# Kernel tuning notes

Hardware: AMD Instinct MI355X
Metric: run time of the kernel (lower is better)

The kernel has to match this reference:

```python
import jax, jax.numpy as jnp
import numpy as np

NUM_HEADS = 2

def mha(q, k, v, w_in, b_in, w_out, b_out):
    # torch nn.MultiheadAttention with batch_first=True, packed in_proj
    E = q.shape[-1]
    Dh = E // NUM_HEADS
    wq, wk, wv = jnp.split(w_in, 3, axis=0)
    bq, bk, bv = jnp.split(b_in, 3, axis=0)
    qh = (q @ wq.T + bq).reshape(q.shape[0], q.shape[1], NUM_HEADS, Dh)
    kh = (k @ wk.T + bk).reshape(k.shape[0], k.shape[1], NUM_HEADS, Dh)
    vh = (v @ wv.T + bv).reshape(v.shape[0], v.shape[1], NUM_HEADS, Dh)
    scores = jnp.einsum('blhd,bmhd->bhlm', qh, kh) / jnp.sqrt(jnp.asarray(Dh, q.dtype))
    attn = jax.nn.softmax(scores, axis=-1)
    ctx = jnp.einsum('bhlm,bmhd->blhd', attn, vh).reshape(q.shape[0], q.shape[1], E)
    return ctx @ w_out.T + b_out


def setup_inputs() -> dict:
    key = jax.random.key(0)
    ks = jax.random.split(key, 10)
    B, S, F, E, H = 16384, 512, 4, 8, 16
    s = 0.3
    return {
        'x': jax.random.normal(ks[0], (B, S, E), jnp.float32),
        'Q': jax.random.normal(ks[1], (F, E), jnp.float32) * s,
        'sa_w_in': jax.random.normal(ks[2], (3 * E, E), jnp.float32) * s,
        'sa_b_in': jnp.zeros((3 * E,), jnp.float32),
        'sa_w_out': jax.random.normal(ks[3], (E, E), jnp.float32) * s,
        'sa_b_out': jnp.zeros((E,), jnp.float32),
        'ca_w_in': jax.random.normal(ks[4], (3 * E, E), jnp.float32) * s,
        'ca_b_in': jnp.zeros((3 * E,), jnp.float32),
        'ca_w_out': jax.random.normal(ks[5], (E, E), jnp.float32) * s,
        'ca_b_out': jnp.zeros((E,), jnp.float32),
        'r_w1': jax.random.normal(ks[6], (H, F * E), jnp.float32) * s,
        'r_b1': jnp.zeros((H,), jnp.float32),
        'r_w2': jax.random.normal(ks[7], (1, H), jnp.float32) * s,
        'r_b2': jnp.zeros((1,), jnp.float32),
    }


def reference(x, Q, sa_w_in, sa_b_in, sa_w_out, sa_b_out,
              ca_w_in, ca_b_in, ca_w_out, ca_b_out,
              r_w1, r_b1, r_w2, r_b2):
    B = x.shape[0]
    # self-attention over the (batch-identical) factor queries
    Qb = jnp.broadcast_to(Q[None], (B,) + Q.shape)  # [B, F, E]
    Q_upd = mha(Qb, Qb, Qb, sa_w_in, sa_b_in, sa_w_out, sa_b_out)
    # cross-attention: factors attend over the input sequence
    Q_cross = mha(Q_upd, x, x, ca_w_in, ca_b_in, ca_w_out, ca_b_out)  # [B, F, E]
    similarity = jnp.einsum('bfe,bse->bfs', Q_cross, x)  # [B, F, S]
    attn_weights = jax.nn.softmax(similarity, axis=-1)
    final_factors = jnp.einsum('bfs,bse->bfe', attn_weights, x)  # [B, F, E]
    fused = final_factors.reshape(B, -1)  # [B, F*E]
    h = jax.nn.relu(fused @ r_w1.T + r_b1)
    out = h @ r_w2.T + r_b2  # [B, 1]
    return out, similarity
```

## Files before the change

### kernel.cpp

```cpp
#include <hip/hip_runtime.h>

#define SEQ 512
#define EMB 8
#define NFAC 4

__global__ void precompute_kernel(
    const float* __restrict__ Q,
    const float* __restrict__ sa_w_in, const float* __restrict__ sa_b_in,
    const float* __restrict__ sa_w_out, const float* __restrict__ sa_b_out,
    const float* __restrict__ ca_w_in, const float* __restrict__ ca_b_in,
    float* __restrict__ ws)
{
    if (threadIdx.x != 0 || blockIdx.x != 0) return;
    float qh[4][8], kh[4][8], vh[4][8];
    for (int l = 0; l < 4; ++l)
        for (int j = 0; j < 8; ++j) {
            float aq = sa_b_in[j], ak = sa_b_in[8 + j], av = sa_b_in[16 + j];
            for (int e = 0; e < 8; ++e) {
                float q = Q[l * 8 + e];
                aq += q * sa_w_in[j * 8 + e];
                ak += q * sa_w_in[(8 + j) * 8 + e];
                av += q * sa_w_in[(16 + j) * 8 + e];
            }
            qh[l][j] = aq; kh[l][j] = ak; vh[l][j] = av;
        }
    float ctxf[4][8];
    for (int h = 0; h < 2; ++h)
        for (int l = 0; l < 4; ++l) {
            float sc[4];
            float mx = -1e30f;
            for (int m = 0; m < 4; ++m) {
                float a = 0.f;
                for (int d = 0; d < 4; ++d) a += qh[l][h*4+d] * kh[m][h*4+d];
                sc[m] = 0.5f * a;
                mx = fmaxf(mx, sc[m]);
            }
            float ssum = 0.f;
            for (int m = 0; m < 4; ++m) { sc[m] = __expf(sc[m] - mx); ssum += sc[m]; }
            for (int d = 0; d < 4; ++d) {
                float a = 0.f;
                for (int m = 0; m < 4; ++m) a += sc[m] * vh[m][h*4+d];
                ctxf[l][h*4+d] = a / ssum;
            }
        }
    float Qu[4][8];
    for (int l = 0; l < 4; ++l)
        for (int e2 = 0; e2 < 8; ++e2) {
            float a = sa_b_out[e2];
            for (int e = 0; e < 8; ++e) a += ctxf[l][e] * sa_w_out[e2 * 8 + e];
            Qu[l][e2] = a;
        }
    float qc[4][8];
    for (int l = 0; l < 4; ++l)
        for (int j = 0; j < 8; ++j) {
            float a = ca_b_in[j];
            for (int e = 0; e < 8; ++e) a += Qu[l][e] * ca_w_in[j * 8 + e];
            qc[l][j] = a;
        }
    for (int h = 0; h < 2; ++h)
        for (int f = 0; f < 4; ++f) {
            int p = h * 4 + f;
            for (int e = 0; e < 8; ++e) {
                float a = 0.f;
                for (int d = 0; d < 4; ++d) a += qc[f][h*4+d] * ca_w_in[(8 + h*4+d) * 8 + e];
                ws[p * 8 + e] = 0.5f * a;
            }
            float a = 0.f;
            for (int d = 0; d < 4; ++d) a += qc[f][h*4+d] * ca_b_in[8 + h*4+d];
            ws[64 + p] = 0.5f * a;
        }
}

__global__ __launch_bounds__(256, 2) void fused_kernel(
    const float* __restrict__ x,
    const float* __restrict__ ca_w_in, const float* __restrict__ ca_b_in,
    const float* __restrict__ ca_w_out, const float* __restrict__ ca_b_out,
    const float* __restrict__ r_w1, const float* __restrict__ r_b1,
    const float* __restrict__ r_w2, const float* __restrict__ r_b2,
    const float* __restrict__ ws,
    float* __restrict__ out, float* __restrict__ sim_out)
{
    const int b = blockIdx.x;
    const int tid = threadIdx.x;
    const int w = __builtin_amdgcn_readfirstlane(tid >> 6);
    const int lane = tid & 63;

    __shared__ float4 sctx4[8];
    __shared__ float sff[4][8];

    const float* xb = x + (size_t)b * (SEQ * EMB);

    const int p0 = 2 * w, p1 = 2 * w + 1;
    const int h = w >> 1;
    float wq0[8], wq1[8], wvv[4][8], bv[4];
    #pragma unroll
    for (int e = 0; e < 8; ++e) { wq0[e] = ws[p0 * 8 + e]; wq1[e] = ws[p1 * 8 + e]; }
    const float cb0 = ws[64 + p0], cb1 = ws[64 + p1];
    #pragma unroll
    for (int d = 0; d < 4; ++d) {
        bv[d] = ca_b_in[16 + h * 4 + d];
        #pragma unroll
        for (int e = 0; e < 8; ++e) wvv[d][e] = ca_w_in[(16 + h * 4 + d) * 8 + e];
    }

    float xr[8][8];
    float acc0[4] = {0.f, 0.f, 0.f, 0.f}, acc1[4] = {0.f, 0.f, 0.f, 0.f};
    float sum0 = 0.f, sum1 = 0.f;
    #pragma unroll
    for (int j = 0; j < 8; ++j) {
        const int s = lane + 64 * j;
        const float4* xp = (const float4*)(xb + s * 8);
        float4 lo = xp[0], hi = xp[1];
        xr[j][0] = lo.x; xr[j][1] = lo.y; xr[j][2] = lo.z; xr[j][3] = lo.w;
        xr[j][4] = hi.x; xr[j][5] = hi.y; xr[j][6] = hi.z; xr[j][7] = hi.w;
        float sc0 = cb0, sc1 = cb1;
        #pragma unroll
        for (int e = 0; e < 8; ++e) { sc0 += wq0[e] * xr[j][e]; sc1 += wq1[e] * xr[j][e]; }
        float e0 = __expf(sc0), e1 = __expf(sc1);
        sum0 += e0; sum1 += e1;
        #pragma unroll
        for (int d = 0; d < 4; ++d) {
            float vh = bv[d];
            #pragma unroll
            for (int e = 0; e < 8; ++e) vh += wvv[d][e] * xr[j][e];
            acc0[d] += e0 * vh;
            acc1[d] += e1 * vh;
        }
    }
    #pragma unroll
    for (int m = 1; m < 64; m <<= 1) {
        sum0 += __shfl_xor(sum0, m, 64);
        sum1 += __shfl_xor(sum1, m, 64);
        #pragma unroll
        for (int d = 0; d < 4; ++d) {
            acc0[d] += __shfl_xor(acc0[d], m, 64);
            acc1[d] += __shfl_xor(acc1[d], m, 64);
        }
    }
    if (lane == 0) {
        float i0 = 1.f / sum0, i1 = 1.f / sum1;
        sctx4[p0] = make_float4(acc0[0] * i0, acc0[1] * i0, acc0[2] * i0, acc0[3] * i0);
        sctx4[p1] = make_float4(acc1[0] * i1, acc1[1] * i1, acc1[2] * i1, acc1[3] * i1);
    }
    __syncthreads();

    float4 c0 = sctx4[w];
    float4 c1 = sctx4[4 + w];
    float qcr[8];
    #pragma unroll
    for (int e = 0; e < 8; ++e) {
        qcr[e] = ca_b_out[e]
            + c0.x * ca_w_out[e*8+0] + c0.y * ca_w_out[e*8+1]
            + c0.z * ca_w_out[e*8+2] + c0.w * ca_w_out[e*8+3]
            + c1.x * ca_w_out[e*8+4] + c1.y * ca_w_out[e*8+5]
            + c1.z * ca_w_out[e*8+6] + c1.w * ca_w_out[e*8+7];
    }

    float facc[8] = {0.f,0.f,0.f,0.f,0.f,0.f,0.f,0.f};
    float fsum = 0.f;
    float* simb = sim_out + (size_t)b * (NFAC * SEQ) + w * SEQ;
    #pragma unroll
    for (int j = 0; j < 8; ++j) {
        const int s = lane + 64 * j;
        float sim = 0.f;
        #pragma unroll
        for (int e = 0; e < 8; ++e) sim += qcr[e] * xr[j][e];
        simb[s] = sim;
        float ez = __expf(sim);
        fsum += ez;
        #pragma unroll
        for (int e = 0; e < 8; ++e) facc[e] += ez * xr[j][e];
    }
    #pragma unroll
    for (int m = 1; m < 64; m <<= 1) {
        fsum += __shfl_xor(fsum, m, 64);
        #pragma unroll
        for (int e = 0; e < 8; ++e) facc[e] += __shfl_xor(facc[e], m, 64);
    }
    if (lane == 0) {
        float inv = 1.f / fsum;
        #pragma unroll
        for (int e = 0; e < 8; ++e) sff[w][e] = facc[e] * inv;
    }
    __syncthreads();

    if (tid < 16) {
        float a = r_b1[tid];
        const float* fusedp = &sff[0][0];
        const float4* w1p = (const float4*)(r_w1 + tid * 32);
        #pragma unroll
        for (int k = 0; k < 8; ++k) {
            float4 ww = w1p[k];
            a += ww.x * fusedp[4*k+0] + ww.y * fusedp[4*k+1]
               + ww.z * fusedp[4*k+2] + ww.w * fusedp[4*k+3];
        }
        a = fmaxf(a, 0.f);
        float v = a * r_w2[tid];
        v += __shfl_xor(v, 1, 64);
        v += __shfl_xor(v, 2, 64);
        v += __shfl_xor(v, 4, 64);
        v += __shfl_xor(v, 8, 64);
        if (tid == 0) out[b] = v + r_b2[0];
    }
}

extern "C" void kernel_launch(void* const* d_in, const int* in_sizes, int n_in,
                              void* d_out, int out_size, void* d_ws, size_t ws_size,
                              hipStream_t stream) {
    const float* x        = (const float*)d_in[0];
    const float* Q        = (const float*)d_in[1];
    const float* sa_w_in  = (const float*)d_in[2];
    const float* sa_b_in  = (const float*)d_in[3];
    const float* sa_w_out = (const float*)d_in[4];
    const float* sa_b_out = (const float*)d_in[5];
    const float* ca_w_in  = (const float*)d_in[6];
    const float* ca_b_in  = (const float*)d_in[7];
    const float* ca_w_out = (const float*)d_in[8];
    const float* ca_b_out = (const float*)d_in[9];
    const float* r_w1     = (const float*)d_in[10];
    const float* r_b1     = (const float*)d_in[11];
    const float* r_w2     = (const float*)d_in[12];
    const float* r_b2     = (const float*)d_in[13];

    float* out = (float*)d_out;
    const int B = in_sizes[0] / (SEQ * EMB);
    float* sim = out + B;
    float* ws  = (float*)d_ws;

    precompute_kernel<<<1, 64, 0, stream>>>(Q, sa_w_in, sa_b_in, sa_w_out, sa_b_out,
                                            ca_w_in, ca_b_in, ws);
    fused_kernel<<<B, 256, 0, stream>>>(x, ca_w_in, ca_b_in, ca_w_out, ca_b_out,
                                        r_w1, r_b1, r_w2, r_b2, ws, out, sim);
}
```

Before: 466.8 us.

## Fold V projection into output projection and parallelize precompute

```diff
diff --git a/kernel.cpp b/kernel.cpp
--- a/kernel.cpp
+++ b/kernel.cpp
@@ -3,78 +3,127 @@
 #define SEQ 512
 #define EMB 8
 #define NFAC 4
+
 
 __global__ void precompute_kernel(
     const float* __restrict__ Q,
     const float* __restrict__ sa_w_in, const float* __restrict__ sa_b_in,
     const float* __restrict__ sa_w_out, const float* __restrict__ sa_b_out,
     const float* __restrict__ ca_w_in, const float* __restrict__ ca_b_in,
+    const float* __restrict__ ca_w_out, const float* __restrict__ ca_b_out,
     float* __restrict__ ws)
 {
-    if (threadIdx.x != 0 || blockIdx.x != 0) return;
-    float qh[4][8], kh[4][8], vh[4][8];
-    for (int l = 0; l < 4; ++l)
-        for (int j = 0; j < 8; ++j) {
-            float aq = sa_b_in[j], ak = sa_b_in[8 + j], av = sa_b_in[16 + j];
-            for (int e = 0; e < 8; ++e) {
-                float q = Q[l * 8 + e];
-                aq += q * sa_w_in[j * 8 + e];
-                ak += q * sa_w_in[(8 + j) * 8 + e];
-                av += q * sa_w_in[(16 + j) * 8 + e];
-            }
-            qh[l][j] = aq; kh[l][j] = ak; vh[l][j] = av;
-        }
-    float ctxf[4][8];
-    for (int h = 0; h < 2; ++h)
-        for (int l = 0; l < 4; ++l) {
-            float sc[4];
-            float mx = -1e30f;
-            for (int m = 0; m < 4; ++m) {
-                float a = 0.f;
-                for (int d = 0; d < 4; ++d) a += qh[l][h*4+d] * kh[m][h*4+d];
-                sc[m] = 0.5f * a;
-                mx = fmaxf(mx, sc[m]);
-            }
-            float ssum = 0.f;
-            for (int m = 0; m < 4; ++m) { sc[m] = __expf(sc[m] - mx); ssum += sc[m]; }
-            for (int d = 0; d < 4; ++d) {
-                float a = 0.f;
-                for (int m = 0; m < 4; ++m) a += sc[m] * vh[m][h*4+d];
-                ctxf[l][h*4+d] = a / ssum;
-            }
-        }
-    float Qu[4][8];
-    for (int l = 0; l < 4; ++l)
-        for (int e2 = 0; e2 < 8; ++e2) {
-            float a = sa_b_out[e2];
-            for (int e = 0; e < 8; ++e) a += ctxf[l][e] * sa_w_out[e2 * 8 + e];
-            Qu[l][e2] = a;
-        }
-    float qc[4][8];
-    for (int l = 0; l < 4; ++l)
-        for (int j = 0; j < 8; ++j) {
-            float a = ca_b_in[j];
-            for (int e = 0; e < 8; ++e) a += Qu[l][e] * ca_w_in[j * 8 + e];
-            qc[l][j] = a;
-        }
-    for (int h = 0; h < 2; ++h)
-        for (int f = 0; f < 4; ++f) {
-            int p = h * 4 + f;
-            for (int e = 0; e < 8; ++e) {
-                float a = 0.f;
-                for (int d = 0; d < 4; ++d) a += qc[f][h*4+d] * ca_w_in[(8 + h*4+d) * 8 + e];
-                ws[p * 8 + e] = 0.5f * a;
-            }
+    const int t = threadIdx.x;
+    __shared__ float sw[608];
+    __shared__ float sqh[32], skh[32], svh[32], sctx[32], sQu[32], sqc[32];
+    enum { OQ = 0, SWIN = 32, SBIN = 224, SWOUT = 248, SBOUT = 312,
+           CWIN = 320, CBIN = 512, CWOUT = 536, CBOUT = 600 };
+
+    for (int i = t; i < 32;  i += 64) sw[OQ + i]    = Q[i];
+    for (int i = t; i < 192; i += 64) sw[SWIN + i]  = sa_w_in[i];
+    for (int i = t; i < 24;  i += 64) sw[SBIN + i]  = sa_b_in[i];
+    for (int i = t; i < 64;  i += 64) sw[SWOUT + i] = sa_w_out[i];
+    if (t < 8) sw[SBOUT + t] = sa_b_out[t];
+    for (int i = t; i < 192; i += 64) sw[CWIN + i]  = ca_w_in[i];
+    for (int i = t; i < 24;  i += 64) sw[CBIN + i]  = ca_b_in[i];
+    for (int i = t; i < 64;  i += 64) sw[CWOUT + i] = ca_w_out[i];
+    if (t < 8) sw[CBOUT + t] = ca_b_out[t];
+    __syncthreads();
+
+    {
+        const int e2 = t >> 3, e = t & 7;
+        float m0 = 0.f, m1 = 0.f;
+        #pragma unroll
+        for (int d = 0; d < 4; ++d) {
+            m0 += sw[CWOUT + e2 * 8 + d]     * sw[CWIN + (16 + d) * 8 + e];
+            m1 += sw[CWOUT + e2 * 8 + 4 + d] * sw[CWIN + (20 + d) * 8 + e];
+        }
+        ws[72 + t]  = m0;
+        ws[136 + t] = m1;
+    }
+    if (t < 8) {
+        float a = sw[CBOUT + t];
+        #pragma unroll
+        for (int d = 0; d < 8; ++d) a += sw[CWOUT + t * 8 + d] * sw[CBIN + 16 + d];
+        ws[200 + t] = a;
+    }
+
+    if (t < 32) {
+        const int l = t >> 3, j = t & 7;
+        float aq = sw[SBIN + j], ak = sw[SBIN + 8 + j], av = sw[SBIN + 16 + j];
+        #pragma unroll
+        for (int e = 0; e < 8; ++e) {
+            const float q = sw[OQ + l * 8 + e];
+            aq += q * sw[SWIN + j * 8 + e];
+            ak += q * sw[SWIN + (8 + j) * 8 + e];
+            av += q * sw[SWIN + (16 + j) * 8 + e];
+        }
+        sqh[t] = aq; skh[t] = ak; svh[t] = av;
+    }
+    __syncthreads();
+
+    if (t < 8) {
+        const int h = t >> 2, l = t & 3;
+        float sc[4], mx = -1e30f;
+        #pragma unroll
+        for (int m = 0; m < 4; ++m) {
             float a = 0.f;
-            for (int d = 0; d < 4; ++d) a += qc[f][h*4+d] * ca_b_in[8 + h*4+d];
-            ws[64 + p] = 0.5f * a;
-        }
+            #pragma unroll
+            for (int d = 0; d < 4; ++d) a += sqh[l * 8 + h * 4 + d] * skh[m * 8 + h * 4 + d];
+            sc[m] = 0.5f * a;
+            mx = fmaxf(mx, sc[m]);
+        }
+        float ssum = 0.f;
+        #pragma unroll
+        for (int m = 0; m < 4; ++m) { sc[m] = __expf(sc[m] - mx); ssum += sc[m]; }
+        const float inv = 1.f / ssum;
+        #pragma unroll
+        for (int d = 0; d < 4; ++d) {
+            float a = 0.f;
+            #pragma unroll
+            for (int m = 0; m < 4; ++m) a += sc[m] * svh[m * 8 + h * 4 + d];
+            sctx[l * 8 + h * 4 + d] = a * inv;
+        }
+    }
+    __syncthreads();
+
+    if (t < 32) {
+        const int l = t >> 3, e2 = t & 7;
+        float a = sw[SBOUT + e2];
+        #pragma unroll
+        for (int e = 0; e < 8; ++e) a += sctx[l * 8 + e] * sw[SWOUT + e2 * 8 + e];
+        sQu[l * 8 + e2] = a;
+    }
+    __syncthreads();
+
+    if (t < 32) {
+        const int l = t >> 3, j = t & 7;
+        float a = sw[CBIN + j];
+        #pragma unroll
+        for (int e = 0; e < 8; ++e) a += sQu[l * 8 + e] * sw[CWIN + j * 8 + e];
+        sqc[l * 8 + j] = a;
+    }
+    __syncthreads();
+
+    {
+        const int p = t >> 3, e = t & 7, h = p >> 2, f = p & 3;
+        float a = 0.f;
+        #pragma unroll
+        for (int d = 0; d < 4; ++d)
+            a += sqc[f * 8 + h * 4 + d] * sw[CWIN + (8 + h * 4 + d) * 8 + e];
+        ws[p * 8 + e] = 0.5f * a;
+    }
+    if (t < 8) {
+        const int p = t, h = p >> 2, f = p & 3;
+        float a = 0.f;
+        #pragma unroll
+        for (int d = 0; d < 4; ++d) a += sqc[f * 8 + h * 4 + d] * sw[CBIN + 8 + h * 4 + d];
+        ws[64 + p] = 0.5f * a;
+    }
 }
 
-__global__ __launch_bounds__(256, 2) void fused_kernel(
+__global__ __launch_bounds__(256, 4) void fused_kernel(
     const float* __restrict__ x,
-    const float* __restrict__ ca_w_in, const float* __restrict__ ca_b_in,
-    const float* __restrict__ ca_w_out, const float* __restrict__ ca_b_out,
     const float* __restrict__ r_w1, const float* __restrict__ r_b1,
     const float* __restrict__ r_w2, const float* __restrict__ r_b2,
     const float* __restrict__ ws,
@@ -85,26 +134,20 @@
     const int w = __builtin_amdgcn_readfirstlane(tid >> 6);
     const int lane = tid & 63;
 
-    __shared__ float4 sctx4[8];
+    __shared__ float4 su4[16];
     __shared__ float sff[4][8];
 
     const float* xb = x + (size_t)b * (SEQ * EMB);
 
     const int p0 = 2 * w, p1 = 2 * w + 1;
-    const int h = w >> 1;
-    float wq0[8], wq1[8], wvv[4][8], bv[4];
+    float wq0[8], wq1[8];
     #pragma unroll
     for (int e = 0; e < 8; ++e) { wq0[e] = ws[p0 * 8 + e]; wq1[e] = ws[p1 * 8 + e]; }
     const float cb0 = ws[64 + p0], cb1 = ws[64 + p1];
-    #pragma unroll
-    for (int d = 0; d < 4; ++d) {
-        bv[d] = ca_b_in[16 + h * 4 + d];
-        #pragma unroll
-        for (int e = 0; e < 8; ++e) wvv[d][e] = ca_w_in[(16 + h * 4 + d) * 8 + e];
-    }
 
     float xr[8][8];
-    float acc0[4] = {0.f, 0.f, 0.f, 0.f}, acc1[4] = {0.f, 0.f, 0.f, 0.f};
+    float xa0[8] = {0.f,0.f,0.f,0.f,0.f,0.f,0.f,0.f};
+    float xa1[8] = {0.f,0.f,0.f,0.f,0.f,0.f,0.f,0.f};
     float sum0 = 0.f, sum1 = 0.f;
     #pragma unroll
     for (int j = 0; j < 8; ++j) {
@@ -116,15 +159,12 @@
         float sc0 = cb0, sc1 = cb1;
         #pragma unroll
         for (int e = 0; e < 8; ++e) { sc0 += wq0[e] * xr[j][e]; sc1 += wq1[e] * xr[j][e]; }
-        float e0 = __expf(sc0), e1 = __expf(sc1);
+        const float e0 = __expf(sc0), e1 = __expf(sc1);
         sum0 += e0; sum1 += e1;
         #pragma unroll
-        for (int d = 0; d < 4; ++d) {
-            float vh = bv[d];
-            #pragma unroll
-            for (int e = 0; e < 8; ++e) vh += wvv[d][e] * xr[j][e];
-            acc0[d] += e0 * vh;
-            acc1[d] += e1 * vh;
+        for (int e = 0; e < 8; ++e) {
+            xa0[e] += e0 * xr[j][e];
+            xa1[e] += e1 * xr[j][e];
         }
     }
     #pragma unroll
@@ -132,29 +172,32 @@
         sum0 += __shfl_xor(sum0, m, 64);
         sum1 += __shfl_xor(sum1, m, 64);
         #pragma unroll
-        for (int d = 0; d < 4; ++d) {
-            acc0[d] += __shfl_xor(acc0[d], m, 64);
-            acc1[d] += __shfl_xor(acc1[d], m, 64);
+        for (int e = 0; e < 8; ++e) {
+            xa0[e] += __shfl_xor(xa0[e], m, 64);
+            xa1[e] += __shfl_xor(xa1[e], m, 64);
         }
     }
     if (lane == 0) {
-        float i0 = 1.f / sum0, i1 = 1.f / sum1;
-        sctx4[p0] = make_float4(acc0[0] * i0, acc0[1] * i0, acc0[2] * i0, acc0[3] * i0);
-        sctx4[p1] = make_float4(acc1[0] * i1, acc1[1] * i1, acc1[2] * i1, acc1[3] * i1);
-    }
-    __syncthreads();
-
-    float4 c0 = sctx4[w];
-    float4 c1 = sctx4[4 + w];
+        const float i0 = 1.f / sum0, i1 = 1.f / sum1;
+        su4[2 * p0]     = make_float4(xa0[0] * i0, xa0[1] * i0, xa0[2] * i0, xa0[3] * i0);
+        su4[2 * p0 + 1] = make_float4(xa0[4] * i0, xa0[5] * i0, xa0[6] * i0, xa0[7] * i0);
+        su4[2 * p1]     = make_float4(xa1[0] * i1, xa1[1] * i1, xa1[2] * i1, xa1[3] * i1);
+        su4[2 * p1 + 1] = make_float4(xa1[4] * i1, xa1[5] * i1, xa1[6] * i1, xa1[7] * i1);
+    }
+    __syncthreads();
+
+    const float* su = (const float*)su4;
+    float u0[8], u1[8];
+    #pragma unroll
+    for (int e = 0; e < 8; ++e) { u0[e] = su[w * 8 + e]; u1[e] = su[(4 + w) * 8 + e]; }
+    const int e2 = lane & 7;
+    float qv = ws[200 + e2];
+    #pragma unroll
+    for (int e = 0; e < 8; ++e)
+        qv += ws[72 + e2 * 8 + e] * u0[e] + ws[136 + e2 * 8 + e] * u1[e];
     float qcr[8];
     #pragma unroll
-    for (int e = 0; e < 8; ++e) {
-        qcr[e] = ca_b_out[e]
-            + c0.x * ca_w_out[e*8+0] + c0.y * ca_w_out[e*8+1]
-            + c0.z * ca_w_out[e*8+2] + c0.w * ca_w_out[e*8+3]
-            + c1.x * ca_w_out[e*8+4] + c1.y * ca_w_out[e*8+5]
-            + c1.z * ca_w_out[e*8+6] + c1.w * ca_w_out[e*8+7];
-    }
+    for (int e = 0; e < 8; ++e) qcr[e] = __shfl(qv, e, 64);
 
     float facc[8] = {0.f,0.f,0.f,0.f,0.f,0.f,0.f,0.f};
     float fsum = 0.f;
@@ -166,7 +209,7 @@
         #pragma unroll
         for (int e = 0; e < 8; ++e) sim += qcr[e] * xr[j][e];
         simb[s] = sim;
-        float ez = __expf(sim);
+        const float ez = __expf(sim);
         fsum += ez;
         #pragma unroll
         for (int e = 0; e < 8; ++e) facc[e] += ez * xr[j][e];
@@ -178,7 +221,7 @@
         for (int e = 0; e < 8; ++e) facc[e] += __shfl_xor(facc[e], m, 64);
     }
     if (lane == 0) {
-        float inv = 1.f / fsum;
+        const float inv = 1.f / fsum;
         #pragma unroll
         for (int e = 0; e < 8; ++e) sff[w][e] = facc[e] * inv;
     }
@@ -191,8 +234,8 @@
         #pragma unroll
         for (int k = 0; k < 8; ++k) {
             float4 ww = w1p[k];
-            a += ww.x * fusedp[4*k+0] + ww.y * fusedp[4*k+1]
-               + ww.z * fusedp[4*k+2] + ww.w * fusedp[4*k+3];
+            a += ww.x * fusedp[4 * k + 0] + ww.y * fusedp[4 * k + 1]
+               + ww.z * fusedp[4 * k + 2] + ww.w * fusedp[4 * k + 3];
         }
         a = fmaxf(a, 0.f);
         float v = a * r_w2[tid];
@@ -228,7 +271,6 @@
     float* ws  = (float*)d_ws;
 
     precompute_kernel<<<1, 64, 0, stream>>>(Q, sa_w_in, sa_b_in, sa_w_out, sa_b_out,
-                                            ca_w_in, ca_b_in, ws);
-    fused_kernel<<<B, 256, 0, stream>>>(x, ca_w_in, ca_b_in, ca_w_out, ca_b_out,
-                                        r_w1, r_b1, r_w2, r_b2, ws, out, sim);
+                                            ca_w_in, ca_b_in, ca_w_out, ca_b_out, ws);
+    fused_kernel<<<B, 256, 0, stream>>>(x, r_w1, r_b1, r_w2, r_b2, ws, out, sim);
 }
```

Measured after the change: 453.5 us. 2.9% less time.
